# Kernel tuning notes

Hardware: AMD Instinct MI355X
Metric: run time of the kernel (lower is better)

## Reference

```python
import jax, jax.numpy as jnp
import numpy as np
import math

N_EMBD = 1024
N_HEAD = 16
B, T = 2, 2048
MASK_VAL = -10.0  # non-standard soft mask value from original module


def setup_inputs() -> dict:
    key = jax.random.key(0)
    k1, k2, k3 = jax.random.split(key, 3)
    scale = 1.0 / math.sqrt(N_EMBD)
    x = jax.random.normal(k1, (B, T, N_EMBD), dtype=jnp.float32)
    # torch Linear weights: (out_features, in_features)
    w_attn = jax.random.normal(k2, (3 * N_EMBD, N_EMBD), dtype=jnp.float32) * scale
    w_proj = jax.random.normal(k3, (N_EMBD, N_EMBD), dtype=jnp.float32) * scale
    return {"x": x, "w_attn": w_attn, "w_proj": w_proj}


def reference(x, w_attn, w_proj):
    Bsz, Tlen, C = x.shape
    hs = C // N_HEAD
    qkv = jnp.einsum('btc,fc->btf', x, w_attn)  # [B,T,3C]
    q, k, v = jnp.split(qkv, 3, axis=-1)
    # [B,H,T,hs]
    q = q.reshape(Bsz, Tlen, N_HEAD, hs).transpose(0, 2, 1, 3)
    k = k.reshape(Bsz, Tlen, N_HEAD, hs).transpose(0, 2, 1, 3)
    v = v.reshape(Bsz, Tlen, N_HEAD, hs).transpose(0, 2, 1, 3)
    att = jnp.einsum('bhqd,bhkd->bhqk', q, k) * (1.0 / math.sqrt(hs))
    causal = jnp.tril(jnp.ones((Tlen, Tlen), dtype=bool))
    att = jnp.where(causal[None, None], att, MASK_VAL)
    att = jax.nn.softmax(att, axis=-1)
    y = jnp.einsum('bhqk,bhkd->bhqd', att, v)
    y = y.transpose(0, 2, 1, 3).reshape(Bsz, Tlen, C)
    return jnp.einsum('btc,fc->btf', y, w_proj)
```

## Files before the change

kernel.cpp:

```cpp
#include <hip/hip_runtime.h>
#include <hip/hip_bf16.h>
#include <stdint.h>

#define BSZ   2
#define TT    2048
#define NH    16
#define HS    64
#define CC    1024
#define C3    3072
#define MT    4096
#define E10   4.5399929762484854e-05f
#define SCL2  0.1803368801111204f

typedef __bf16 bf16;
typedef __bf16 bf16x8 __attribute__((ext_vector_type(8)));
typedef float  f32x4  __attribute__((ext_vector_type(4)));
typedef short  s16x4  __attribute__((ext_vector_type(4)));

#define AS1 __attribute__((address_space(1)))
#define AS3 __attribute__((address_space(3)))

__device__ __forceinline__ void glds16(const bf16* g, bf16* l) {
    __builtin_amdgcn_global_load_lds((const AS1 void*)g, (AS3 void*)l, 16, 0, 0);
}

__global__ void detect_dtype(const uint16_t* __restrict__ x, int* __restrict__ flag) {
    __shared__ int cnt;
    if (threadIdx.x == 0) cnt = 0;
    __syncthreads();
    int local = 0;
    for (int i = threadIdx.x; i < 512; i += 256) {
        uint16_t u = x[i];
        int e = (u >> 7) & 0xFF;
        if (e >= 96 && e <= 159) local++;
    }
    atomicAdd(&cnt, local);
    __syncthreads();
    if (threadIdx.x == 0) *flag = (cnt >= 461) ? 0 : 1;
}

#define NX8  (MT * CC / 8)
#define NWA8 (C3 * CC / 8)
#define NWP8 (CC * CC / 8)
__global__ __launch_bounds__(256)
void convert_all(const float* __restrict__ x, const float* __restrict__ wa,
                 const float* __restrict__ wp, bf16* __restrict__ xd,
                 bf16* __restrict__ wad, bf16* __restrict__ wpd,
                 const int* __restrict__ flag) {
    if (*flag == 0) return;
    long i = (long)blockIdx.x * 256 + threadIdx.x;
    const float* s; bf16* d; long off;
    if (i < NX8)             { s = x;  d = xd;  off = i; }
    else if (i < NX8 + NWA8) { s = wa; d = wad; off = i - NX8; }
    else                     { s = wp; d = wpd; off = i - NX8 - NWA8; }
    const float4* sp = reinterpret_cast<const float4*>(s) + off * 2;
    float4 a = sp[0], b = sp[1];
    bf16x8 r;
    r[0] = (bf16)a.x; r[1] = (bf16)a.y; r[2] = (bf16)a.z; r[3] = (bf16)a.w;
    r[4] = (bf16)b.x; r[5] = (bf16)b.y; r[6] = (bf16)b.z; r[7] = (bf16)b.w;
    reinterpret_cast<bf16x8*>(d)[off] = r;
}

__global__ __launch_bounds__(256)
void gemm_bt(const bf16* __restrict__ A0, const bf16* __restrict__ A1,
             const bf16* __restrict__ B0, const bf16* __restrict__ B1,
             void* __restrict__ Cmain, bf16* __restrict__ Cv,
             const int* __restrict__ flag,
             int M, int N, int K, int lda, int ldb, int ldc,
             int split_col, int cf32_dyn) {
    __shared__ bf16 As[2][128 * 32];
    __shared__ bf16 Bs[2][128 * 32];

    const int f = *flag;
    const bf16* A = f ? A1 : A0;
    const bf16* B = f ? B1 : B0;
    const int cf32 = cf32_dyn & f;

    const int tid  = threadIdx.x;
    const int lane = tid & 63;
    const int wave = tid >> 6;
    const int wm   = wave >> 1;
    const int wn   = wave & 1;
    const int quad = lane >> 4;
    const int l16  = lane & 15;

    const int row0 = blockIdx.y * 128;
    const int col0 = blockIdx.x * 128;

    const int srow = tid >> 2;
    const int skk  = (tid & 3) * 8;

    const bf16* Ap = A + (long)(row0 + srow) * lda + skk;
    const bf16* Bp = B + (long)(col0 + srow) * ldb + skk;

    auto stage = [&](int k0, int buf) {
        glds16(Ap + k0,                  &As[buf][wave * 512]);
        glds16(Ap + (long)64 * lda + k0, &As[buf][wave * 512 + 2048]);
        glds16(Bp + k0,                  &Bs[buf][wave * 512]);
        glds16(Bp + (long)64 * ldb + k0, &Bs[buf][wave * 512 + 2048]);
    };

    f32x4 acc[4][4] = {};
    stage(0, 0);

    for (int k0 = 0; k0 < K; k0 += 32) {
        const int buf = (k0 >> 5) & 1;
        __syncthreads();
        if (k0 + 32 < K) stage(k0 + 32, buf ^ 1);

        const bf16* Ac = As[buf];
        const bf16* Bc = Bs[buf];
        bf16x8 af[4], bfv[4];
#pragma unroll
        for (int mi = 0; mi < 4; ++mi)
            af[mi] = *reinterpret_cast<const bf16x8*>(&Ac[(wm * 64 + mi * 16 + l16) * 32 + quad * 8]);
#pragma unroll
        for (int ni = 0; ni < 4; ++ni)
            bfv[ni] = *reinterpret_cast<const bf16x8*>(&Bc[(wn * 64 + ni * 16 + l16) * 32 + quad * 8]);
#pragma unroll
        for (int mi = 0; mi < 4; ++mi)
#pragma unroll
            for (int ni = 0; ni < 4; ++ni)
                acc[mi][ni] = __builtin_amdgcn_mfma_f32_16x16x32_bf16(af[mi], bfv[ni], acc[mi][ni], 0, 0, 0);
    }

    if (split_col < 0 || col0 < split_col) {
#pragma unroll
        for (int mi = 0; mi < 4; ++mi)
#pragma unroll
            for (int ni = 0; ni < 4; ++ni)
#pragma unroll
                for (int r = 0; r < 4; ++r) {
                    int row = row0 + wm * 64 + mi * 16 + quad * 4 + r;
                    int col = col0 + wn * 64 + ni * 16 + l16;
                    float v = acc[mi][ni][r];
                    if (cf32) ((float*)Cmain)[(long)row * ldc + col] = v;
                    else      ((bf16*)Cmain)[(long)row * ldc + col] = (bf16)v;
                }
    } else {
        const int h  = (col0 - split_col + wn * 64) >> 6;
        const int bq = row0 >> 11;
        const int tc = ((row0 & 2047) >> 6) + wm;
#pragma unroll
        for (int ni = 0; ni < 4; ++ni) {
            long vrow = (long)(bq * NH + h) * 64 + ni * 16 + l16;
#pragma unroll
            for (int mi = 0; mi < 4; ++mi) {
                bf16 outv[4];
#pragma unroll
                for (int r = 0; r < 4; ++r) outv[r] = (bf16)acc[mi][ni][r];
                *reinterpret_cast<uint2*>(&Cv[vrow * 2048 + tc * 64 + quad * 16 + mi * 4]) =
                    *reinterpret_cast<uint2*>(outv);
            }
        }
    }
}

__global__ __launch_bounds__(256)
void gemm_bt64(const bf16* __restrict__ A0, const bf16* __restrict__ A1,
               const bf16* __restrict__ B0, const bf16* __restrict__ B1,
               void* __restrict__ C, const int* __restrict__ flag,
               int M, int N, int K, int lda, int ldb, int ldc, int cf32_dyn) {
    __shared__ bf16 As[2][128 * 32];
    __shared__ bf16 Bs[2][64 * 32];

    const int f = *flag;
    const bf16* A = f ? A1 : A0;
    const bf16* B = f ? B1 : B0;
    const int cf32 = cf32_dyn & f;

    const int tid  = threadIdx.x;
    const int lane = tid & 63;
    const int wave = tid >> 6;
    const int wm   = wave >> 1;
    const int wn   = wave & 1;
    const int quad = lane >> 4;
    const int l16  = lane & 15;

    const int row0 = blockIdx.y * 128;
    const int col0 = blockIdx.x * 64;

    const int srow = tid >> 2;
    const int skk  = (tid & 3) * 8;

    const bf16* Ap = A + (long)(row0 + srow) * lda + skk;
    const bf16* Bp = B + (long)(col0 + srow) * ldb + skk;

    auto stage = [&](int k0, int buf) {
        glds16(Ap + k0,                  &As[buf][wave * 512]);
        glds16(Ap + (long)64 * lda + k0, &As[buf][wave * 512 + 2048]);
        glds16(Bp + k0,                  &Bs[buf][wave * 512]);
    };

    f32x4 acc[4][2] = {};
    stage(0, 0);

    for (int k0 = 0; k0 < K; k0 += 32) {
        const int buf = (k0 >> 5) & 1;
        __syncthreads();
        if (k0 + 32 < K) stage(k0 + 32, buf ^ 1);

        const bf16* Ac = As[buf];
        const bf16* Bc = Bs[buf];
        bf16x8 af[4], bfv[2];
#pragma unroll
        for (int mi = 0; mi < 4; ++mi)
            af[mi] = *reinterpret_cast<const bf16x8*>(&Ac[(wm * 64 + mi * 16 + l16) * 32 + quad * 8]);
#pragma unroll
        for (int ni = 0; ni < 2; ++ni)
            bfv[ni] = *reinterpret_cast<const bf16x8*>(&Bc[(wn * 32 + ni * 16 + l16) * 32 + quad * 8]);
#pragma unroll
        for (int mi = 0; mi < 4; ++mi)
#pragma unroll
            for (int ni = 0; ni < 2; ++ni)
                acc[mi][ni] = __builtin_amdgcn_mfma_f32_16x16x32_bf16(af[mi], bfv[ni], acc[mi][ni], 0, 0, 0);
    }

#pragma unroll
    for (int mi = 0; mi < 4; ++mi)
#pragma unroll
        for (int ni = 0; ni < 2; ++ni)
#pragma unroll
            for (int r = 0; r < 4; ++r) {
                int row = row0 + wm * 64 + mi * 16 + quad * 4 + r;
                int col = col0 + wn * 32 + ni * 16 + l16;
                float v = acc[mi][ni][r];
                if (cf32) ((float*)C)[(long)row * ldc + col] = v;
                else      ((bf16*)C)[(long)row * ldc + col] = (bf16)v;
            }
}

__global__ __launch_bounds__(256)
void vtile2(const bf16* __restrict__ Vt, float* __restrict__ Vtile) {
    const int kt = blockIdx.x, bh = blockIdx.y;
    const int tid = threadIdx.x;
    const int d = tid >> 2, part = tid & 3;
    const bf16* p = Vt + ((long)bh * 64 + d) * 2048 + kt * 64 + part * 16;
    float s = 0.f;
#pragma unroll
    for (int i = 0; i < 2; ++i) {
        bf16x8 v = *reinterpret_cast<const bf16x8*>(p + i * 8);
#pragma unroll
        for (int j = 0; j < 8; ++j) s += (float)v[j];
    }
    s += __shfl_xor(s, 1, 64);
    s += __shfl_xor(s, 2, 64);
    if (part == 0) Vtile[((long)bh * 32 + kt) * 64 + d] = s;
}

__global__ void vts_suffix(const float* __restrict__ Vtile, float* __restrict__ Vts) {
    const int bh = blockIdx.x, d = threadIdx.x;
    Vts[((long)bh * 33 + 32) * 64 + d] = 0.f;
    float acc = 0.f;
    for (int kt = 31; kt >= 0; --kt) {
        acc += Vtile[((long)bh * 32 + kt) * 64 + d];
        Vts[((long)bh * 33 + kt) * 64 + d] = acc;
    }
}

__global__ __launch_bounds__(256, 3)
void attn(bf16* __restrict__ qk, const bf16* __restrict__ Vt,
          const float* __restrict__ Vts) {
    __shared__ bf16 Ks[3][64 * 64];
    __shared__ bf16 Vs[3][64 * 64];

    const int tid  = threadIdx.x;
    const int lane = tid & 63;
    const int wave = tid >> 6;
    const int quad = lane >> 4;
    const int l16  = lane & 15;

    const int f2   = blockIdx.x;
    const int xcd  = f2 & 7;
    const int slot = f2 >> 3;
    const int u    = slot & 3;
    const int chunk = 31 - (slot >> 2);
    const int h = xcd * 2 + (u & 1);
    const int b = u >> 1;
    const int bh = b * 16 + h;
    const int q0 = chunk * 64;
    const long rbase = (long)b * TT;
    const int ktend = chunk + 1;

    const bf16* qp = qk + (rbase + q0 + wave * 16 + l16) * 2048 + h * HS;
    bf16x8 qf0 = *reinterpret_cast<const bf16x8*>(qp + quad * 8);
    bf16x8 qf1 = *reinterpret_cast<const bf16x8*>(qp + 32 + quad * 8);

    f32x4 O[4] = {};
    float lp = 0.f;

    const int rl  = lane >> 3;
    const int cs  = (lane & 7) ^ rl;
    const int row0dma = wave * 16 + rl;
    const bf16* kgb = qk + (rbase + row0dma) * 2048 + CC + h * HS + cs * 8;
    const bf16* vgb = Vt + ((long)(b * NH + h) * 64 + row0dma) * 2048 + cs * 8;
    const int sx = l16 & 7;

    auto stage = [&](int kt, int buf) {
        glds16(kgb + (long)(kt * 64) * 2048,     &Ks[buf][wave * 1024]);
        glds16(kgb + (long)(kt * 64 + 8) * 2048, &Ks[buf][wave * 1024 + 512]);
        glds16(vgb + kt * 64,                    &Vs[buf][wave * 1024]);
        glds16(vgb + 8 * 2048 + kt * 64,         &Vs[buf][wave * 1024 + 512]);
    };

    stage(0, 0);
    stage(ktend > 1 ? 1 : 0, 1);

    int rb = 0;
    int sb = 2;
    for (int kt = 0; kt < ktend; ++kt) {
        asm volatile("s_waitcnt vmcnt(4)" ::: "memory");
        __builtin_amdgcn_s_barrier();
        __builtin_amdgcn_sched_barrier(0);

        int nkt = kt + 2; nkt = (nkt < ktend) ? nkt : (ktend - 1);
        stage(nkt, sb);

        const bf16* Kc = Ks[rb];
        const bf16* Vc = Vs[rb];

        bf16x8 kf0[4], kf1[4];
#pragma unroll
        for (int g = 0; g < 4; ++g) {
            const int krow = g * 16 + l16;
            kf0[g] = *reinterpret_cast<const bf16x8*>(&Kc[krow * 64 + ((quad ^ sx) * 8)]);
            kf1[g] = *reinterpret_cast<const bf16x8*>(&Kc[krow * 64 + (((4 + quad) ^ sx) * 8)]);
        }
        s16x4 vf[4][4];
#pragma unroll
        for (int dg = 0; dg < 4; ++dg) {
            const int vrow = dg * 16 + l16;
            union { uint4 u; s16x4 s[2]; } ua, ub;
            ua.u = *reinterpret_cast<const uint4*>(&Vc[vrow * 64 + (((2 * quad) ^ sx) * 8)]);
            ub.u = *reinterpret_cast<const uint4*>(&Vc[vrow * 64 + (((2 * quad + 1) ^ sx) * 8)]);
            vf[dg][0] = ua.s[0]; vf[dg][1] = ua.s[1];
            vf[dg][2] = ub.s[0]; vf[dg][3] = ub.s[1];
        }

        f32x4 S[4] = {};
        __builtin_amdgcn_s_setprio(1);
#pragma unroll
        for (int g = 0; g < 4; ++g) {
            S[g] = __builtin_amdgcn_mfma_f32_16x16x32_bf16(kf0[g], qf0, S[g], 0, 0, 0);
            S[g] = __builtin_amdgcn_mfma_f32_16x16x32_bf16(kf1[g], qf1, S[g], 0, 0, 0);
        }
        __builtin_amdgcn_s_setprio(0);

        const bool dtile = (kt == ktend - 1);
        const int ql = wave * 16 + l16;
        s16x4 pk[4];
#pragma unroll
        for (int g = 0; g < 4; ++g) {
#pragma unroll
            for (int r = 0; r < 4; ++r) {
                float p = __builtin_exp2f(S[g][r] * SCL2);
                if (dtile) {
                    int kl = g * 16 + quad * 4 + r;
                    p = (kl > ql) ? E10 : p;
                }
                lp += p;
                union { bf16 b_; short s_; } u2;
                u2.b_ = (bf16)p;
                pk[g][r] = u2.s_;
            }
        }

        __builtin_amdgcn_s_setprio(1);
#pragma unroll
        for (int dg = 0; dg < 4; ++dg) {
            O[dg] = __builtin_amdgcn_mfma_f32_16x16x16bf16_1k(vf[dg][0], pk[0], O[dg], 0, 0, 0);
            O[dg] = __builtin_amdgcn_mfma_f32_16x16x16bf16_1k(vf[dg][1], pk[1], O[dg], 0, 0, 0);
            O[dg] = __builtin_amdgcn_mfma_f32_16x16x16bf16_1k(vf[dg][2], pk[2], O[dg], 0, 0, 0);
            O[dg] = __builtin_amdgcn_mfma_f32_16x16x16bf16_1k(vf[dg][3], pk[3], O[dg], 0, 0, 0);
        }
        __builtin_amdgcn_s_setprio(0);

        rb = (rb == 2) ? 0 : rb + 1;
        sb = (sb == 2) ? 0 : sb + 1;
    }

    lp += __shfl_xor(lp, 16, 64);
    lp += __shfl_xor(lp, 32, 64);

    const int nfut = TT - ktend * 64;
    const float l = lp + (float)nfut * E10;
    const float invl = 1.0f / l;
    const float* vfp = Vts + ((long)bh * 33 + ktend) * 64;

    bf16* yp = qk + (rbase + q0 + wave * 16 + l16) * 2048 + h * HS;
#pragma unroll
    for (int dg = 0; dg < 4; ++dg) {
        bf16 outv[4];
#pragma unroll
        for (int r = 0; r < 4; ++r) {
            float o = O[dg][r] + E10 * vfp[dg * 16 + quad * 4 + r];
            outv[r] = (bf16)(o * invl);
        }
        *reinterpret_cast<uint2*>(yp + dg * 16 + quad * 4) =
            *reinterpret_cast<uint2*>(outv);
    }
}

extern "C" void kernel_launch(void* const* d_in, const int* in_sizes, int n_in,
                              void* d_out, int out_size, void* d_ws, size_t ws_size,
                              hipStream_t stream) {
    const void* x      = d_in[0];
    const void* w_attn = d_in[1];
    const void* w_proj = d_in[2];

    char* ws = (char*)d_ws;
    bf16*  qk     = (bf16*)ws;
    bf16*  Vt     = (bf16*)(ws + (size_t)MT * 2048 * 2);
    char*  p2     = ws + (size_t)MT * 2048 * 2 + (size_t)32 * 64 * 2048 * 2;
    int*   flag   = (int*)p2;
    float* Vts    = (float*)(p2 + 256);
    bf16*  wp_cvt = (bf16*)(p2 + 256 + 32 * 33 * 64 * 4);
    float* Vtile  = (float*)((char*)wp_cvt + (size_t)CC * CC * 2);

    bf16* x_cvt  = (bf16*)d_out;
    bf16* wa_cvt = (bf16*)d_out + (size_t)MT * CC;

    detect_dtype<<<1, 256, 0, stream>>>((const uint16_t*)x, flag);
    convert_all<<<(NX8 + NWA8 + NWP8) / 256, 256, 0, stream>>>(
        (const float*)x, (const float*)w_attn, (const float*)w_proj,
        x_cvt, wa_cvt, wp_cvt, flag);

    gemm_bt<<<dim3(C3 / 128, MT / 128), 256, 0, stream>>>(
        (const bf16*)x, x_cvt, (const bf16*)w_attn, wa_cvt, qk, Vt, flag,
        MT, C3, CC, CC, CC, 2048, 2048, 0);

    vtile2<<<dim3(32, BSZ * NH), 256, 0, stream>>>(Vt, Vtile);
    vts_suffix<<<dim3(BSZ * NH), dim3(64), 0, stream>>>(Vtile, Vts);

    attn<<<dim3(1024), 256, 0, stream>>>(qk, Vt, Vts);

    gemm_bt64<<<dim3(CC / 64, MT / 128), 256, 0, stream>>>(
        qk, qk, (const bf16*)w_proj, wp_cvt, d_out, flag,
        MT, CC, CC, 2048, CC, CC, 1);
}
```

Before: 185.7 us.

## Split attention key tiles across waves with cross-wave LDS reduction

Each wave now takes a 16-key slice of every K/V tile for all 64 queries, where before each wave handled 16 queries against all 64 keys. Partial outputs and row sums are combined across waves through shared memory at the end. Buffering drops from triple to double with __syncthreads, and the occupancy hint drops from 3 to 2 blocks. This cuts per-wave LDS fragment reads of K, but raises register use (16 accumulators), adds an end-of-kernel reduction, and weakens load/compute overlap.

```diff
diff --git a/kernel.cpp b/kernel.cpp
--- a/kernel.cpp
+++ b/kernel.cpp
@@ -258,15 +258,14 @@
     }
 }
 
-__global__ __launch_bounds__(256, 3)
+__global__ __launch_bounds__(256, 2)
 void attn(bf16* __restrict__ qk, const bf16* __restrict__ Vt,
           const float* __restrict__ Vts) {
-    __shared__ bf16 Ks[3][64 * 64];
-    __shared__ bf16 Vs[3][64 * 64];
+    __shared__ __align__(16) char smem[52224];
 
     const int tid  = threadIdx.x;
     const int lane = tid & 63;
-    const int wave = tid >> 6;
+    const int w    = tid >> 6;
     const int quad = lane >> 4;
     const int l16  = lane & 15;
 
@@ -282,118 +281,153 @@
     const long rbase = (long)b * TT;
     const int ktend = chunk + 1;
 
-    const bf16* qp = qk + (rbase + q0 + wave * 16 + l16) * 2048 + h * HS;
-    bf16x8 qf0 = *reinterpret_cast<const bf16x8*>(qp + quad * 8);
-    bf16x8 qf1 = *reinterpret_cast<const bf16x8*>(qp + 32 + quad * 8);
-
-    f32x4 O[4] = {};
-    float lp = 0.f;
+    bf16x8 qf[4][2];
+#pragma unroll
+    for (int qg = 0; qg < 4; ++qg) {
+        const bf16* qp = qk + (rbase + q0 + qg * 16 + l16) * 2048 + h * HS;
+        qf[qg][0] = *reinterpret_cast<const bf16x8*>(qp + quad * 8);
+        qf[qg][1] = *reinterpret_cast<const bf16x8*>(qp + 32 + quad * 8);
+    }
+
+    f32x4 O[4][4] = {};
+    float lp[4] = {};
 
     const int rl  = lane >> 3;
     const int cs  = (lane & 7) ^ rl;
-    const int row0dma = wave * 16 + rl;
+    const int row0dma = w * 16 + rl;
     const bf16* kgb = qk + (rbase + row0dma) * 2048 + CC + h * HS + cs * 8;
     const bf16* vgb = Vt + ((long)(b * NH + h) * 64 + row0dma) * 2048 + cs * 8;
     const int sx = l16 & 7;
 
-    auto stage = [&](int kt, int buf) {
-        glds16(kgb + (long)(kt * 64) * 2048,     &Ks[buf][wave * 1024]);
-        glds16(kgb + (long)(kt * 64 + 8) * 2048, &Ks[buf][wave * 1024 + 512]);
-        glds16(vgb + kt * 64,                    &Vs[buf][wave * 1024]);
-        glds16(vgb + 8 * 2048 + kt * 64,         &Vs[buf][wave * 1024 + 512]);
+    auto KsB = [&](int bi) { return (bf16*)(smem + bi * 8192); };
+    auto VsB = [&](int bi) { return (bf16*)(smem + 16384 + bi * 8192); };
+
+    auto stage = [&](int kt, int bi) {
+        glds16(kgb + (long)(kt * 64) * 2048,     KsB(bi) + w * 1024);
+        glds16(kgb + (long)(kt * 64 + 8) * 2048, KsB(bi) + w * 1024 + 512);
+        glds16(vgb + kt * 64,                    VsB(bi) + w * 1024);
+        glds16(vgb + 8 * 2048 + kt * 64,         VsB(bi) + w * 1024 + 512);
     };
 
     stage(0, 0);
-    stage(ktend > 1 ? 1 : 0, 1);
-
-    int rb = 0;
-    int sb = 2;
+
     for (int kt = 0; kt < ktend; ++kt) {
-        asm volatile("s_waitcnt vmcnt(4)" ::: "memory");
-        __builtin_amdgcn_s_barrier();
-        __builtin_amdgcn_sched_barrier(0);
-
-        int nkt = kt + 2; nkt = (nkt < ktend) ? nkt : (ktend - 1);
-        stage(nkt, sb);
-
-        const bf16* Kc = Ks[rb];
-        const bf16* Vc = Vs[rb];
-
-        bf16x8 kf0[4], kf1[4];
-#pragma unroll
-        for (int g = 0; g < 4; ++g) {
-            const int krow = g * 16 + l16;
-            kf0[g] = *reinterpret_cast<const bf16x8*>(&Kc[krow * 64 + ((quad ^ sx) * 8)]);
-            kf1[g] = *reinterpret_cast<const bf16x8*>(&Kc[krow * 64 + (((4 + quad) ^ sx) * 8)]);
-        }
-        s16x4 vf[4][4];
+        const int buf = kt & 1;
+        __syncthreads();
+        if (kt + 1 < ktend) stage(kt + 1, buf ^ 1);
+
+        const bf16* Kc = KsB(buf);
+        const bf16* Vc = VsB(buf);
+
+        const bf16x8 kf0 = *reinterpret_cast<const bf16x8*>(
+            &Kc[(w * 16 + l16) * 64 + ((quad ^ sx) * 8)]);
+        const bf16x8 kf1 = *reinterpret_cast<const bf16x8*>(
+            &Kc[(w * 16 + l16) * 64 + (((4 + quad) ^ sx) * 8)]);
+
+        s16x4 vf[4];
 #pragma unroll
         for (int dg = 0; dg < 4; ++dg) {
             const int vrow = dg * 16 + l16;
-            union { uint4 u; s16x4 s[2]; } ua, ub;
-            ua.u = *reinterpret_cast<const uint4*>(&Vc[vrow * 64 + (((2 * quad) ^ sx) * 8)]);
-            ub.u = *reinterpret_cast<const uint4*>(&Vc[vrow * 64 + (((2 * quad + 1) ^ sx) * 8)]);
-            vf[dg][0] = ua.s[0]; vf[dg][1] = ua.s[1];
-            vf[dg][2] = ub.s[0]; vf[dg][3] = ub.s[1];
+            union { uint4 u4; s16x4 s[2]; } ua, ub;
+            ua.u4 = *reinterpret_cast<const uint4*>(&Vc[vrow * 64 + (((2 * quad) ^ sx) * 8)]);
+            ub.u4 = *reinterpret_cast<const uint4*>(&Vc[vrow * 64 + (((2 * quad + 1) ^ sx) * 8)]);
+            if      (w == 0) vf[dg] = ua.s[0];
+            else if (w == 1) vf[dg] = ua.s[1];
+            else if (w == 2) vf[dg] = ub.s[0];
+            else             vf[dg] = ub.s[1];
         }
 
         f32x4 S[4] = {};
         __builtin_amdgcn_s_setprio(1);
 #pragma unroll
-        for (int g = 0; g < 4; ++g) {
-            S[g] = __builtin_amdgcn_mfma_f32_16x16x32_bf16(kf0[g], qf0, S[g], 0, 0, 0);
-            S[g] = __builtin_amdgcn_mfma_f32_16x16x32_bf16(kf1[g], qf1, S[g], 0, 0, 0);
+        for (int qg = 0; qg < 4; ++qg) {
+            S[qg] = __builtin_amdgcn_mfma_f32_16x16x32_bf16(kf0, qf[qg][0], S[qg], 0, 0, 0);
+            S[qg] = __builtin_amdgcn_mfma_f32_16x16x32_bf16(kf1, qf[qg][1], S[qg], 0, 0, 0);
         }
         __builtin_amdgcn_s_setprio(0);
 
         const bool dtile = (kt == ktend - 1);
-        const int ql = wave * 16 + l16;
+        const int klbase = w * 16 + quad * 4;
         s16x4 pk[4];
 #pragma unroll
-        for (int g = 0; g < 4; ++g) {
+        for (int qg = 0; qg < 4; ++qg) {
 #pragma unroll
             for (int r = 0; r < 4; ++r) {
-                float p = __builtin_exp2f(S[g][r] * SCL2);
+                float p = __builtin_exp2f(S[qg][r] * SCL2);
                 if (dtile) {
-                    int kl = g * 16 + quad * 4 + r;
+                    int kl = klbase + r;
+                    int ql = qg * 16 + l16;
                     p = (kl > ql) ? E10 : p;
                 }
-                lp += p;
+                lp[qg] += p;
                 union { bf16 b_; short s_; } u2;
                 u2.b_ = (bf16)p;
-                pk[g][r] = u2.s_;
+                pk[qg][r] = u2.s_;
             }
         }
 
         __builtin_amdgcn_s_setprio(1);
 #pragma unroll
-        for (int dg = 0; dg < 4; ++dg) {
-            O[dg] = __builtin_amdgcn_mfma_f32_16x16x16bf16_1k(vf[dg][0], pk[0], O[dg], 0, 0, 0);
-            O[dg] = __builtin_amdgcn_mfma_f32_16x16x16bf16_1k(vf[dg][1], pk[1], O[dg], 0, 0, 0);
-            O[dg] = __builtin_amdgcn_mfma_f32_16x16x16bf16_1k(vf[dg][2], pk[2], O[dg], 0, 0, 0);
-            O[dg] = __builtin_amdgcn_mfma_f32_16x16x16bf16_1k(vf[dg][3], pk[3], O[dg], 0, 0, 0);
-        }
+        for (int dg = 0; dg < 4; ++dg)
+#pragma unroll
+            for (int qg = 0; qg < 4; ++qg)
+                O[dg][qg] = __builtin_amdgcn_mfma_f32_16x16x16bf16_1k(
+                    vf[dg], pk[qg], O[dg][qg], 0, 0, 0);
         __builtin_amdgcn_s_setprio(0);
-
-        rb = (rb == 2) ? 0 : rb + 1;
-        sb = (sb == 2) ? 0 : sb + 1;
-    }
-
-    lp += __shfl_xor(lp, 16, 64);
-    lp += __shfl_xor(lp, 32, 64);
+    }
+
+#pragma unroll
+    for (int qg = 0; qg < 4; ++qg) {
+        lp[qg] += __shfl_xor(lp[qg], 16, 64);
+        lp[qg] += __shfl_xor(lp[qg], 32, 64);
+    }
+
+    __syncthreads();
+    f32x4* redO = (f32x4*)smem;
+    float* redL = (float*)(smem + 49152);
+
+#pragma unroll
+    for (int qg = 0; qg < 4; ++qg) {
+        if (qg != w) {
+            const int k = (w - qg - 1) & 3;
+#pragma unroll
+            for (int dg = 0; dg < 4; ++dg)
+                redO[((qg * 3 + k) * 4 + dg) * 64 + lane] = O[dg][qg];
+            if (quad == 0) redL[(qg * 3 + k) * 64 + l16] = lp[qg];
+        }
+    }
+    __syncthreads();
+
+    f32x4 Of[4] = {};
+    float lpf = 0.f;
+#pragma unroll
+    for (int qg = 0; qg < 4; ++qg) {
+        if (qg == w) {
+#pragma unroll
+            for (int dg = 0; dg < 4; ++dg) Of[dg] += O[dg][qg];
+            lpf += lp[qg];
+        }
+    }
+#pragma unroll
+    for (int k = 0; k < 3; ++k) {
+#pragma unroll
+        for (int dg = 0; dg < 4; ++dg)
+            Of[dg] += redO[((w * 3 + k) * 4 + dg) * 64 + lane];
+        lpf += redL[(w * 3 + k) * 64 + l16];
+    }
 
     const int nfut = TT - ktend * 64;
-    const float l = lp + (float)nfut * E10;
+    const float l = lpf + (float)nfut * E10;
     const float invl = 1.0f / l;
     const float* vfp = Vts + ((long)bh * 33 + ktend) * 64;
 
-    bf16* yp = qk + (rbase + q0 + wave * 16 + l16) * 2048 + h * HS;
+    bf16* yp = qk + (rbase + q0 + w * 16 + l16) * 2048 + h * HS;
 #pragma unroll
     for (int dg = 0; dg < 4; ++dg) {
         bf16 outv[4];
 #pragma unroll
         for (int r = 0; r < 4; ++r) {
-            float o = O[dg][r] + E10 * vfp[dg * 16 + quad * 4 + r];
+            float o = Of[dg][r] + E10 * vfp[dg * 16 + quad * 4 + r];
             outv[r] = (bf16)(o * invl);
         }
         *reinterpret_cast<uint2*>(yp + dg * 16 + quad * 4) =
```

New measurement: 187.5 us. About the same (+1.0%).
